# Kernel tuning notes

Measured on AMD Instinct MI355X. Metric: run time of the kernel, lower is better.

Reference implementation:

```python
import jax, jax.numpy as jnp
import numpy as np

BATCH, NUM_MASKS, IN_DIM, OUT_DIM = 512, 16, 1024, 1024


def setup_inputs() -> dict:
    key = jax.random.key(0)
    k1, k2, k3 = jax.random.split(key, 3)
    x = jax.random.normal(k1, (BATCH, NUM_MASKS, IN_DIM), dtype=jnp.float32)
    kernel = jax.random.normal(k2, (IN_DIM, OUT_DIM), dtype=jnp.float32) * (1.0 / np.sqrt(IN_DIM))
    masks = jax.random.uniform(k3, (NUM_MASKS, IN_DIM, OUT_DIM), dtype=jnp.float32)
    return {"x": x, "kernel": kernel, "masks": masks}


def reference(x, kernel, masks):
    # masked_kernel[m, i, o] = kernel[i, o] * masks[m, i, o]
    masked_kernel = kernel[None, :, :] * masks  # (M, I, O)
    # Original tf.scan serializes batch; equivalent math is one batched einsum:
    # out[b, m, o] = sum_i x[b, m, i] * masked_kernel[m, i, o]
    # NOTE: the executed tf.scan path applies NO activation, so neither do we.
    out = jnp.einsum('bmi,mio->bmo', x, masked_kernel)  # (B, M, O)
    return out
```

## Files before the change

### kernel.cpp

```cpp
#include <hip/hip_runtime.h>
#include <hip/hip_bf16.h>


#define BATCH 512
#define NMASK 16
#define IN_D  1024
#define OUT_D 1024

#define BM 128
#define BN 128
#define BK 32
#define NT (IN_D / BK)
#define AKP 40
#define BKP 34
#define MFSZ (BK * BN)
#define THREADS 512

using bf16x8 = __attribute__((ext_vector_type(8))) __bf16;
using bf16x4 = __attribute__((ext_vector_type(4))) __bf16;
using f32x4  = __attribute__((ext_vector_type(4))) float;
using f32x2  = __attribute__((ext_vector_type(2))) float;

typedef const __attribute__((address_space(1))) void gvoid_t;
typedef __attribute__((address_space(3))) void lvoid_t;

__device__ __forceinline__ void dma16(const void* g, const void* l) {
    __builtin_amdgcn_global_load_lds((gvoid_t*)(uintptr_t)g,
                                     (lvoid_t*)(uintptr_t)l, 16, 0, 0);
}

__global__ void __launch_bounds__(THREADS, 4)
mdl_mfma_kernel(const float* __restrict__ X,
                const float* __restrict__ Kn,
                const float* __restrict__ Mk,
                float* __restrict__ Out)
{
    __shared__ __align__(16) float          Mf[3 * MFSZ];
    __shared__ __align__(16) unsigned short As[BM * AKP];
    __shared__ __align__(16) unsigned short Bs[BN * BKP];

    const int t = threadIdx.x;
    const int l = t & 63;
    const int w = t >> 6;

    const int raw = blockIdx.x;
    const int wg  = (raw & 7) * 64 + (raw >> 3);
    const int m   = wg >> 5;
    const int ob  = (wg >> 2) & 7;
    const int bb  = wg & 3;

    const int wr = w >> 2;
    const int wc = w & 3;

    f32x4 acc[4][2];
#pragma unroll
    for (int mi = 0; mi < 4; ++mi)
#pragma unroll
        for (int ni = 0; ni < 2; ++ni)
            acc[mi][ni] = (f32x4){0.f, 0.f, 0.f, 0.f};

    const int a_row = t >> 2;
    const int a_kh  = (t & 3) * 8;
    const int o2 = (t & 63) * 2;
    const int k4 = w * 4;

    const int obase = ob * BN;
    const float* Xa  = X + ((size_t)(bb * BM + a_row) * NMASK + m) * IN_D + a_kh;
    const float* Knb = Kn + obase + o2;
    const float* Mkm = Mk + (size_t)m * IN_D * OUT_D;

    auto DMA = [&](int tile, int c) {
        const int kt = tile * BK;
#pragma unroll
        for (int j = 0; j < 2; ++j) {
            const int k = j * 16 + w * 2 + (l >> 5);
            const float* gsrc = Mkm + (size_t)(kt + k) * OUT_D + obase + (l & 31) * 4;
            const float* ldst = &Mf[c * MFSZ + j * 2048 + w * 256];
            dma16(gsrc, ldst);
        }
    };

    auto MFMA_PHASE = [&]() {
        const int kg = (l >> 4) * 8;
        bf16x8 bfv[2];
#pragma unroll
        for (int ni = 0; ni < 2; ++ni) {
            const int n = wc * 32 + ni * 16 + (l & 15);
            bf16x4 lo = *(const bf16x4*)(&Bs[n * BKP + kg]);
            bf16x4 hi = *(const bf16x4*)(&Bs[n * BKP + kg + 4]);
            bf16x8 f;
            f[0] = lo[0]; f[1] = lo[1]; f[2] = lo[2]; f[3] = lo[3];
            f[4] = hi[0]; f[5] = hi[1]; f[6] = hi[2]; f[7] = hi[3];
            bfv[ni] = f;
        }
#pragma unroll
        for (int mi = 0; mi < 4; ++mi) {
            const int r = wr * 64 + mi * 16 + (l & 15);
            bf16x8 af = *(const bf16x8*)(&As[r * AKP + kg]);
#pragma unroll
            for (int ni = 0; ni < 2; ++ni)
                acc[mi][ni] = __builtin_amdgcn_mfma_f32_16x16x32_bf16(
                    af, bfv[ni], acc[mi][ni], 0, 0, 0);
        }
    };

    DMA(0, 0);
    DMA(1, 1);
    asm volatile("s_waitcnt vmcnt(2)" ::: "memory");
    __builtin_amdgcn_sched_barrier(0);
    __builtin_amdgcn_s_barrier();
    __builtin_amdgcn_sched_barrier(0);

    int c_cur = 0, c_nxt = 1, c_far = 2;

    for (int tt = 0; tt < NT; ++tt) {
        const int kt = tt * BK;

        f32x4 xv0 = *(const f32x4*)(Xa + kt);
        f32x4 xv1 = *(const f32x4*)(Xa + kt + 4);
        f32x2 kv[4];
#pragma unroll
        for (int r = 0; r < 4; ++r)
            kv[r] = *(const f32x2*)(Knb + (size_t)(kt + k4 + r) * OUT_D);
        __builtin_amdgcn_sched_barrier(0);

        const int tile_pf = (tt + 2 < NT) ? (tt + 2) : 0;
        DMA(tile_pf, c_far);
        __builtin_amdgcn_sched_barrier(0);

        {
            f32x2 mvv[4];
#pragma unroll
            for (int r = 0; r < 4; ++r)
                mvv[r] = *(const f32x2*)(&Mf[c_cur * MFSZ + (k4 + r) * BN + o2]);
#pragma unroll
            for (int c = 0; c < 2; ++c) {
                bf16x4 v;
#pragma unroll
                for (int r = 0; r < 4; ++r)
                    v[r] = (__bf16)(kv[r][c] * mvv[r][c]);
                *(bf16x4*)(&Bs[(o2 + c) * BKP + k4]) = v;
            }
            bf16x8 va;
#pragma unroll
            for (int j = 0; j < 4; ++j) {
                va[j]     = (__bf16)xv0[j];
                va[4 + j] = (__bf16)xv1[j];
            }
            *(bf16x8*)(&As[a_row * AKP + a_kh]) = va;
        }

        asm volatile("s_waitcnt lgkmcnt(0)" ::: "memory");
        __builtin_amdgcn_sched_barrier(0);
        __builtin_amdgcn_s_barrier();
        __builtin_amdgcn_sched_barrier(0);

        __builtin_amdgcn_s_setprio(1);
        MFMA_PHASE();
        __builtin_amdgcn_s_setprio(0);

        asm volatile("s_waitcnt vmcnt(2)" ::: "memory");
        __builtin_amdgcn_sched_barrier(0);
        __builtin_amdgcn_s_barrier();
        __builtin_amdgcn_sched_barrier(0);

        const int tmp = c_cur; c_cur = c_nxt; c_nxt = c_far; c_far = tmp;
    }

    asm volatile("s_waitcnt vmcnt(0)" ::: "memory");

    const int r0 = bb * BM + wr * 64 + (l >> 4) * 4;
    const int c0 = ob * BN + wc * 32 + (l & 15);
#pragma unroll
    for (int mi = 0; mi < 4; ++mi) {
#pragma unroll
        for (int j = 0; j < 4; ++j) {
            const size_t row = (size_t)(r0 + mi * 16 + j);
            float* op = Out + (row * NMASK + m) * OUT_D + c0;
#pragma unroll
            for (int ni = 0; ni < 2; ++ni)
                op[ni * 16] = acc[mi][ni][j];
        }
    }
}

extern "C" void kernel_launch(void* const* d_in, const int* in_sizes, int n_in,
                              void* d_out, int out_size, void* d_ws, size_t ws_size,
                              hipStream_t stream) {
    (void)in_sizes; (void)n_in; (void)d_ws; (void)ws_size; (void)out_size;
    const float* X  = (const float*)d_in[0];
    const float* Kn = (const float*)d_in[1];
    const float* Mk = (const float*)d_in[2];
    float* Out = (float*)d_out;

    const int nblocks = (BATCH / BM) * (OUT_D / BN) * NMASK;
    mdl_mfma_kernel<<<nblocks, THREADS, 0, stream>>>(X, Kn, Mk, Out);
}
```

Measured before the change: 52.45 us.

## Split masked-weight prep into a separate bf16 pre-pass feeding a BK=64 GEMM

Adds a prep kernel that computes kernel*mask once per (mask, in, out) element and writes it to workspace as bf16 in a tile-blocked layout. The GEMM kernel then DMAs that pre-swizzled bf16 tile straight into LDS with K=64 per step, and double-buffers the X conversion. Before, each of the four batch blocks recomputed the masked product and read the fp32 masks. The new path adds a second launch and a round trip of the 32MB bf16 weight through global memory. The old fused kernel stays as a fallback when the workspace is too small.

```diff
diff --git a/kernel.cpp b/kernel.cpp
--- a/kernel.cpp
+++ b/kernel.cpp
@@ -9,17 +9,16 @@
 
 #define BM 128
 #define BN 128
-#define BK 32
+#define BK 64
 #define NT (IN_D / BK)
-#define AKP 40
-#define BKP 34
-#define MFSZ (BK * BN)
+#define TILE_ELEMS (BN * BK)
 #define THREADS 512
 
 using bf16x8 = __attribute__((ext_vector_type(8))) __bf16;
 using bf16x4 = __attribute__((ext_vector_type(4))) __bf16;
 using f32x4  = __attribute__((ext_vector_type(4))) float;
 using f32x2  = __attribute__((ext_vector_type(2))) float;
+using u16x4  = __attribute__((ext_vector_type(4))) unsigned short;
 
 typedef const __attribute__((address_space(1))) void gvoid_t;
 typedef __attribute__((address_space(3))) void lvoid_t;
@@ -30,14 +29,50 @@
 }
 
 __global__ void __launch_bounds__(THREADS, 4)
-mdl_mfma_kernel(const float* __restrict__ X,
-                const float* __restrict__ Kn,
-                const float* __restrict__ Mk,
-                float* __restrict__ Out)
+mdl_prep_w(const float* __restrict__ Kn,
+           const float* __restrict__ Mk,
+           unsigned short* __restrict__ Wt)
 {
-    __shared__ __align__(16) float          Mf[3 * MFSZ];
-    __shared__ __align__(16) unsigned short As[BM * AKP];
-    __shared__ __align__(16) unsigned short Bs[BN * BKP];
+    const int t = threadIdx.x;
+    const int l = t & 63;
+    const int w = t >> 6;
+
+    const int raw = blockIdx.x;
+    const int wg  = (raw & 7) * 256 + (raw >> 3);
+    const int m   = wg >> 7;
+    const int ob  = (wg >> 4) & 7;
+    const int k2  = wg & 15;
+
+    const int i0 = k2 * 64 + w * 8;
+    const int o0 = ob * BN + 2 * l;
+
+    const float* mkb = Mk + ((size_t)m * IN_D + i0) * OUT_D + o0;
+    const float* knb = Kn + (size_t)i0 * OUT_D + o0;
+
+    f32x2 a[8], b[8];
+#pragma unroll
+    for (int r = 0; r < 8; ++r) {
+        a[r] = *(const f32x2*)(mkb + (size_t)r * OUT_D);
+        b[r] = *(const f32x2*)(knb + (size_t)r * OUT_D);
+    }
+    bf16x8 g0, g1;
+#pragma unroll
+    for (int r = 0; r < 8; ++r) {
+        g0[r] = (__bf16)(a[r][0] * b[r][0]);
+        g1[r] = (__bf16)(a[r][1] * b[r][1]);
+    }
+    unsigned short* dst = Wt + (size_t)wg * TILE_ELEMS + t * 16;
+    *(bf16x8*)(dst)     = g0;
+    *(bf16x8*)(dst + 8) = g1;
+}
+
+__global__ void __launch_bounds__(THREADS, 4)
+mdl_gemm(const float* __restrict__ X,
+         const unsigned short* __restrict__ Wt,
+         float* __restrict__ Out)
+{
+    __shared__ __align__(16) unsigned short As[2][TILE_ELEMS];
+    __shared__ __align__(16) unsigned short Bs[3][TILE_ELEMS];
 
     const int t = threadIdx.x;
     const int l = t & 63;
@@ -49,8 +84,150 @@
     const int ob  = (wg >> 2) & 7;
     const int bb  = wg & 3;
 
-    const int wr = w >> 2;
-    const int wc = w & 3;
+    const int wr = w >> 2, wc = w & 3;
+
+    f32x4 acc[4][2];
+#pragma unroll
+    for (int mi = 0; mi < 4; ++mi)
+#pragma unroll
+        for (int ni = 0; ni < 2; ++ni)
+            acc[mi][ni] = (f32x4){0.f, 0.f, 0.f, 0.f};
+
+    const int a_row = t >> 2;
+    const int a_g0  = (t & 3) * 2;
+    const float* Xa = X + ((size_t)(bb * BM + a_row) * NMASK + m) * IN_D + (t & 3) * 16;
+
+    const unsigned short* Wb = Wt + (size_t)(m * 8 + ob) * NT * TILE_ELEMS;
+
+    auto DMAB = [&](int tile, int c) {
+#pragma unroll
+        for (int j = 0; j < 2; ++j) {
+            const unsigned short* src =
+                Wb + (size_t)tile * TILE_ELEMS + (size_t)(j * 512 + w * 64 + l) * 8;
+            dma16(src, &Bs[c][j * 4096 + w * 512]);
+        }
+    };
+
+    f32x4 xv0, xv1, xv2, xv3;
+
+    auto LOADX = [&](int kt) {
+        xv0 = *(const f32x4*)(Xa + kt);
+        xv1 = *(const f32x4*)(Xa + kt + 4);
+        xv2 = *(const f32x4*)(Xa + kt + 8);
+        xv3 = *(const f32x4*)(Xa + kt + 12);
+    };
+    auto STORE_A = [&](int buf) {
+        bf16x8 v0, v1;
+#pragma unroll
+        for (int j = 0; j < 4; ++j) {
+            v0[j] = (__bf16)xv0[j]; v0[4 + j] = (__bf16)xv1[j];
+            v1[j] = (__bf16)xv2[j]; v1[4 + j] = (__bf16)xv3[j];
+        }
+        unsigned short* p = &As[buf][a_g0 * 1024 + a_row * 8];
+        *(bf16x8*)p          = v0;
+        *(bf16x8*)(p + 1024) = v1;
+    };
+    auto MFMAP = [&](int abuf, int bc) {
+#pragma unroll
+        for (int s = 0; s < 2; ++s) {
+            const int gs = s * 4 + (l >> 4);
+            bf16x8 bfv[2];
+#pragma unroll
+            for (int ni = 0; ni < 2; ++ni)
+                bfv[ni] = *(const bf16x8*)
+                    &Bs[bc][gs * 1024 + (wc * 32 + ni * 16 + (l & 15)) * 8];
+#pragma unroll
+            for (int mi = 0; mi < 4; ++mi) {
+                bf16x8 af = *(const bf16x8*)
+                    &As[abuf][gs * 1024 + (wr * 64 + mi * 16 + (l & 15)) * 8];
+#pragma unroll
+                for (int ni = 0; ni < 2; ++ni)
+                    acc[mi][ni] = __builtin_amdgcn_mfma_f32_16x16x32_bf16(
+                        af, bfv[ni], acc[mi][ni], 0, 0, 0);
+            }
+        }
+    };
+
+    LOADX(0);
+    __builtin_amdgcn_sched_barrier(0);
+    DMAB(0, 0);
+    DMAB(1, 1);
+    __builtin_amdgcn_sched_barrier(0);
+    STORE_A(0);
+    asm volatile("s_waitcnt lgkmcnt(0)" ::: "memory");
+    __builtin_amdgcn_sched_barrier(0);
+    asm volatile("s_waitcnt vmcnt(2)" ::: "memory");
+    __builtin_amdgcn_sched_barrier(0);
+    __builtin_amdgcn_s_barrier();
+    __builtin_amdgcn_sched_barrier(0);
+
+    int c_cur = 0, c_nxt = 1, c_far = 2;
+
+    for (int tt = 0; tt < NT; ++tt) {
+        if (tt + 1 < NT) {
+            LOADX((tt + 1) * BK);
+            __builtin_amdgcn_sched_barrier(0);
+        }
+        DMAB((tt + 2 < NT) ? tt + 2 : 0, c_far);
+        __builtin_amdgcn_sched_barrier(0);
+
+        __builtin_amdgcn_s_setprio(1);
+        MFMAP(tt & 1, c_cur);
+        __builtin_amdgcn_s_setprio(0);
+
+        if (tt + 1 < NT) STORE_A((tt + 1) & 1);
+
+        asm volatile("s_waitcnt lgkmcnt(0)" ::: "memory");
+        __builtin_amdgcn_sched_barrier(0);
+        asm volatile("s_waitcnt vmcnt(2)" ::: "memory");
+        __builtin_amdgcn_sched_barrier(0);
+        __builtin_amdgcn_s_barrier();
+        __builtin_amdgcn_sched_barrier(0);
+
+        const int tmp = c_cur; c_cur = c_nxt; c_nxt = c_far; c_far = tmp;
+    }
+    asm volatile("s_waitcnt vmcnt(0)" ::: "memory");
+
+    const int r0 = bb * BM + wr * 64 + (l >> 4) * 4;
+    const int c0 = ob * BN + wc * 32 + (l & 15);
+#pragma unroll
+    for (int mi = 0; mi < 4; ++mi) {
+#pragma unroll
+        for (int j = 0; j < 4; ++j) {
+            const size_t row = (size_t)(r0 + mi * 16 + j);
+            float* op = Out + (row * NMASK + m) * OUT_D + c0;
+#pragma unroll
+            for (int ni = 0; ni < 2; ++ni)
+                op[ni * 16] = acc[mi][ni][j];
+        }
+    }
+}
+
+#define FAKP 40
+#define FBKP 34
+#define FMFSZ (32 * BN)
+
+__global__ void __launch_bounds__(THREADS, 4)
+mdl_fused_fallback(const float* __restrict__ X,
+                   const float* __restrict__ Kn,
+                   const float* __restrict__ Mk,
+                   float* __restrict__ Out)
+{
+    __shared__ __align__(16) float          Mf[3 * FMFSZ];
+    __shared__ __align__(16) unsigned short As[BM * FAKP];
+    __shared__ __align__(16) unsigned short Bs[BN * FBKP];
+
+    const int t = threadIdx.x;
+    const int l = t & 63;
+    const int w = t >> 6;
+
+    const int raw = blockIdx.x;
+    const int wg  = (raw & 7) * 64 + (raw >> 3);
+    const int m   = wg >> 5;
+    const int ob  = (wg >> 2) & 7;
+    const int bb  = wg & 3;
+
+    const int wr = w >> 2, wc = w & 3;
 
     f32x4 acc[4][2];
 #pragma unroll
@@ -70,37 +247,12 @@
     const float* Mkm = Mk + (size_t)m * IN_D * OUT_D;
 
     auto DMA = [&](int tile, int c) {
-        const int kt = tile * BK;
+        const int kt = tile * 32;
 #pragma unroll
         for (int j = 0; j < 2; ++j) {
             const int k = j * 16 + w * 2 + (l >> 5);
             const float* gsrc = Mkm + (size_t)(kt + k) * OUT_D + obase + (l & 31) * 4;
-            const float* ldst = &Mf[c * MFSZ + j * 2048 + w * 256];
-            dma16(gsrc, ldst);
-        }
-    };
-
-    auto MFMA_PHASE = [&]() {
-        const int kg = (l >> 4) * 8;
-        bf16x8 bfv[2];
-#pragma unroll
-        for (int ni = 0; ni < 2; ++ni) {
-            const int n = wc * 32 + ni * 16 + (l & 15);
-            bf16x4 lo = *(const bf16x4*)(&Bs[n * BKP + kg]);
-            bf16x4 hi = *(const bf16x4*)(&Bs[n * BKP + kg + 4]);
-            bf16x8 f;
-            f[0] = lo[0]; f[1] = lo[1]; f[2] = lo[2]; f[3] = lo[3];
-            f[4] = hi[0]; f[5] = hi[1]; f[6] = hi[2]; f[7] = hi[3];
-            bfv[ni] = f;
-        }
-#pragma unroll
-        for (int mi = 0; mi < 4; ++mi) {
-            const int r = wr * 64 + mi * 16 + (l & 15);
-            bf16x8 af = *(const bf16x8*)(&As[r * AKP + kg]);
-#pragma unroll
-            for (int ni = 0; ni < 2; ++ni)
-                acc[mi][ni] = __builtin_amdgcn_mfma_f32_16x16x32_bf16(
-                    af, bfv[ni], acc[mi][ni], 0, 0, 0);
+            dma16(gsrc, &Mf[c * FMFSZ + j * 2048 + w * 256]);
         }
     };
 
@@ -113,9 +265,8 @@
 
     int c_cur = 0, c_nxt = 1, c_far = 2;
 
-    for (int tt = 0; tt < NT; ++tt) {
-        const int kt = tt * BK;
-
+    for (int tt = 0; tt < 32; ++tt) {
+        const int kt = tt * 32;
         f32x4 xv0 = *(const f32x4*)(Xa + kt);
         f32x4 xv1 = *(const f32x4*)(Xa + kt + 4);
         f32x2 kv[4];
@@ -123,50 +274,61 @@
         for (int r = 0; r < 4; ++r)
             kv[r] = *(const f32x2*)(Knb + (size_t)(kt + k4 + r) * OUT_D);
         __builtin_amdgcn_sched_barrier(0);
-
-        const int tile_pf = (tt + 2 < NT) ? (tt + 2) : 0;
-        DMA(tile_pf, c_far);
-        __builtin_amdgcn_sched_barrier(0);
-
+        DMA((tt + 2 < 32) ? tt + 2 : 0, c_far);
+        __builtin_amdgcn_sched_barrier(0);
         {
             f32x2 mvv[4];
 #pragma unroll
             for (int r = 0; r < 4; ++r)
-                mvv[r] = *(const f32x2*)(&Mf[c_cur * MFSZ + (k4 + r) * BN + o2]);
+                mvv[r] = *(const f32x2*)(&Mf[c_cur * FMFSZ + (k4 + r) * BN + o2]);
 #pragma unroll
             for (int c = 0; c < 2; ++c) {
                 bf16x4 v;
 #pragma unroll
                 for (int r = 0; r < 4; ++r)
                     v[r] = (__bf16)(kv[r][c] * mvv[r][c]);
-                *(bf16x4*)(&Bs[(o2 + c) * BKP + k4]) = v;
+                *(bf16x4*)(&Bs[(o2 + c) * FBKP + k4]) = v;
             }
             bf16x8 va;
 #pragma unroll
             for (int j = 0; j < 4; ++j) {
-                va[j]     = (__bf16)xv0[j];
-                va[4 + j] = (__bf16)xv1[j];
-            }
-            *(bf16x8*)(&As[a_row * AKP + a_kh]) = va;
-        }
-
+                va[j] = (__bf16)xv0[j]; va[4 + j] = (__bf16)xv1[j];
+            }
+            *(bf16x8*)(&As[a_row * FAKP + a_kh]) = va;
+        }
         asm volatile("s_waitcnt lgkmcnt(0)" ::: "memory");
         __builtin_amdgcn_sched_barrier(0);
         __builtin_amdgcn_s_barrier();
         __builtin_amdgcn_sched_barrier(0);
-
-        __builtin_amdgcn_s_setprio(1);
-        MFMA_PHASE();
-        __builtin_amdgcn_s_setprio(0);
-
+        {
+            const int kg = (l >> 4) * 8;
+            bf16x8 bfv[2];
+#pragma unroll
+            for (int ni = 0; ni < 2; ++ni) {
+                const int n = wc * 32 + ni * 16 + (l & 15);
+                bf16x4 lo = *(const bf16x4*)(&Bs[n * FBKP + kg]);
+                bf16x4 hi = *(const bf16x4*)(&Bs[n * FBKP + kg + 4]);
+                bf16x8 f;
+                f[0] = lo[0]; f[1] = lo[1]; f[2] = lo[2]; f[3] = lo[3];
+                f[4] = hi[0]; f[5] = hi[1]; f[6] = hi[2]; f[7] = hi[3];
+                bfv[ni] = f;
+            }
+#pragma unroll
+            for (int mi = 0; mi < 4; ++mi) {
+                const int r = wr * 64 + mi * 16 + (l & 15);
+                bf16x8 af = *(const bf16x8*)(&As[r * FAKP + kg]);
+#pragma unroll
+                for (int ni = 0; ni < 2; ++ni)
+                    acc[mi][ni] = __builtin_amdgcn_mfma_f32_16x16x32_bf16(
+                        af, bfv[ni], acc[mi][ni], 0, 0, 0);
+            }
+        }
         asm volatile("s_waitcnt vmcnt(2)" ::: "memory");
         __builtin_amdgcn_sched_barrier(0);
         __builtin_amdgcn_s_barrier();
         __builtin_amdgcn_sched_barrier(0);
-
         const int tmp = c_cur; c_cur = c_nxt; c_nxt = c_far; c_far = tmp;
     }
-
     asm volatile("s_waitcnt vmcnt(0)" ::: "memory");
 
     const int r0 = bb * BM + wr * 64 + (l >> 4) * 4;
@@ -187,12 +349,17 @@
 extern "C" void kernel_launch(void* const* d_in, const int* in_sizes, int n_in,
                               void* d_out, int out_size, void* d_ws, size_t ws_size,
                               hipStream_t stream) {
-    (void)in_sizes; (void)n_in; (void)d_ws; (void)ws_size; (void)out_size;
+    (void)in_sizes; (void)n_in; (void)out_size;
     const float* X  = (const float*)d_in[0];
     const float* Kn = (const float*)d_in[1];
     const float* Mk = (const float*)d_in[2];
     float* Out = (float*)d_out;
 
-    const int nblocks = (BATCH / BM) * (OUT_D / BN) * NMASK;
-    mdl_mfma_kernel<<<nblocks, THREADS, 0, stream>>>(X, Kn, Mk, Out);
-}
+    if (ws_size >= (size_t)NMASK * IN_D * OUT_D * sizeof(unsigned short)) {
+        unsigned short* Wt = (unsigned short*)d_ws;
+        mdl_prep_w<<<NMASK * 8 * NT, THREADS, 0, stream>>>(Kn, Mk, Wt);
+        mdl_gemm<<<(BATCH / BM) * (OUT_D / BN) * NMASK, THREADS, 0, stream>>>(X, Wt, Out);
+    } else {
+        mdl_fused_fallback<<<512, THREADS, 0, stream>>>(X, Kn, Mk, Out);
+    }
+}
```

After: 59.45 us. 1.13x slower.
